# Optimization experiments

Measured on AMD Instinct MI355X. Metric: run time of the kernel, lower is better.

The kernel has to match this reference:

```python
import jax, jax.numpy as jnp
import numpy as np

B, N, H, FE = 1024, 128, 128, 8  # jets batch, particles per jet, hidden, features+1


def setup_inputs() -> dict:
    key = jax.random.key(0)
    ks = jax.random.split(key, 6)
    s = 0.05  # small init scale to keep gates in a sane range
    return {
        "h": jax.random.normal(ks[0], (B, N, H), dtype=jnp.float32),
        "jets": jax.random.normal(ks[1], (B, N, FE), dtype=jnp.float32),
        "mask": jnp.ones((B, N), dtype=bool),  # unused by MPIdentity.forward, kept for signature parity
        "Wm": jax.random.normal(ks[2], (H, H), dtype=jnp.float32) * s,
        "bm": jnp.zeros((H,), dtype=jnp.float32),
        "W_ih": jax.random.normal(ks[3], (3 * H, H + FE), dtype=jnp.float32) * s,
        "W_hh": jax.random.normal(ks[4], (3 * H, H), dtype=jnp.float32) * s,
        "b_ih": jnp.zeros((3 * H,), dtype=jnp.float32),
        "b_hh": jnp.zeros((3 * H,), dtype=jnp.float32),
    }


def reference(h, jets, mask, Wm, bm, W_ih, W_hh, b_ih, b_hh):
    # DTNNMessage: linear hidden->hidden (nn.Linear applies x @ W.T + b)
    msg = jnp.einsum("bnh,kh->bnk", h, Wm) + bm            # [B,N,H]
    # sum over particles, broadcast back (repeat), tanh activation
    dist = jnp.sum(msg, axis=1, keepdims=True)              # [B,1,H]
    message = jnp.tanh(jnp.broadcast_to(dist, h.shape))     # [B,N,H]
    # GRUUpdate: GRUCell on concat([message, jets]) with state h
    x = jnp.concatenate([message, jets], axis=-1)           # [B,N,H+FE]
    gi = jnp.einsum("bnf,gf->bng", x, W_ih) + b_ih          # [B,N,3H]
    gh = jnp.einsum("bnh,gh->bng", h, W_hh) + b_hh          # [B,N,3H]
    i_r, i_z, i_n = jnp.split(gi, 3, axis=-1)
    h_r, h_z, h_n = jnp.split(gh, 3, axis=-1)
    r = jax.nn.sigmoid(i_r + h_r)
    z = jax.nn.sigmoid(i_z + h_z)
    n = jnp.tanh(i_n + r * h_n)
    return (1.0 - z) * n + z * h                            # [B,N,H]
```

## Files before the change

### kernel.cpp

```cpp
#include <hip/hip_runtime.h>
#include <hip/hip_bf16.h>

#define B_   1024
#define N_   128
#define H_   128
#define FE_  8
#define G3_  384

typedef short s8v __attribute__((ext_vector_type(8)));
typedef float f4v __attribute__((ext_vector_type(4)));

__device__ __forceinline__ unsigned short f2bf(float x) {
    unsigned int u = __float_as_uint(x);
    u += 0x7fffu + ((u >> 16) & 1u);
    return (unsigned short)(u >> 16);
}
__device__ __forceinline__ float bf2f(unsigned short s) {
    return __uint_as_float(((unsigned int)s) << 16);
}

__global__ __launch_bounds__(256) void k1_prep(
    const float* __restrict__ h, const float* __restrict__ Wm,
    const float* __restrict__ bm, const float* __restrict__ W_ih,
    const float* __restrict__ W_hh, const float* __restrict__ b_ih,
    float* __restrict__ gi_base,
    unsigned short* __restrict__ Whi, unsigned short* __restrict__ Wlo,
    unsigned short* __restrict__ Wth, unsigned short* __restrict__ Wtl)
{
    const int b = blockIdx.x;
    const int t = threadIdx.x;

    if (t < 51) {
        const int i = b * 51 + t;
        if (i < 49152) {
            const float x = W_hh[i];
            const unsigned short hb = f2bf(x);
            Whi[i] = hb;
            Wlo[i] = f2bf(x - bf2f(hb));
        } else {
            const int j = i - 49152;
            const float x = W_ih[(j >> 3) * 136 + 128 + (j & 7)];
            const unsigned short hb = f2bf(x);
            Wth[j] = hb;
            Wtl[j] = f2bf(x - bf2f(hb));
        }
    }

    __shared__ __align__(16) float4 part[256];
    __shared__ __align__(16) float  hsum[H_];
    __shared__ __align__(16) float  msg[H_];

    const float4* h4 = reinterpret_cast<const float4*>(h + (size_t)b * (N_ * H_));
    const int kc = t & 31;
    const int ng = t >> 5;
    float4 s = make_float4(0.f, 0.f, 0.f, 0.f);
    #pragma unroll
    for (int i = 0; i < 16; ++i) {
        float4 v = h4[(ng * 16 + i) * 32 + kc];
        s.x += v.x; s.y += v.y; s.z += v.z; s.w += v.w;
    }
    part[t] = s;
    __syncthreads();
    if (t < 32) {
        float4 a = part[t];
        #pragma unroll
        for (int g = 1; g < 8; ++g) {
            float4 v = part[g * 32 + t];
            a.x += v.x; a.y += v.y; a.z += v.z; a.w += v.w;
        }
        reinterpret_cast<float4*>(hsum)[t] = a;
    }
    __syncthreads();

    if (t < H_) {
        const float4* wr  = reinterpret_cast<const float4*>(Wm + t * H_);
        const float4* hs4 = reinterpret_cast<const float4*>(hsum);
        float d = 0.f;
        #pragma unroll
        for (int j = 0; j < 32; ++j) {
            float4 w = wr[j]; float4 x = hs4[j];
            d += w.x * x.x + w.y * x.y + w.z * x.z + w.w * x.w;
        }
        d += (float)N_ * bm[t];
        msg[t] = tanhf(d);
    }
    __syncthreads();

    for (int g = t; g < G3_; g += 256) {
        const float4* wr = reinterpret_cast<const float4*>(W_ih + g * (H_ + FE_));
        const float4* m4 = reinterpret_cast<const float4*>(msg);
        float d = 0.f;
        #pragma unroll
        for (int j = 0; j < 32; ++j) {
            float4 w = wr[j]; float4 x = m4[j];
            d += w.x * x.x + w.y * x.y + w.z * x.z + w.w * x.w;
        }
        gi_base[b * G3_ + g] = d + b_ih[g];
    }
}

__global__ __launch_bounds__(512, 4) void k2_mfma(
    const float* __restrict__ h, const float* __restrict__ jets,
    const unsigned short* __restrict__ Whi, const unsigned short* __restrict__ Wlo,
    const unsigned short* __restrict__ Wth, const unsigned short* __restrict__ Wtl,
    const float* __restrict__ b_hh, const float* __restrict__ gi_base,
    float* __restrict__ out)
{
    __shared__ __align__(16) unsigned short Ah[64 * H_];
    __shared__ __align__(16) unsigned short Al[64 * H_];

    const int t    = threadIdx.x;
    const int row0 = blockIdx.x * 64;
    const int b    = row0 >> 7;
    const int wv   = t >> 6;
    const int l    = t & 63;
    const int lr   = l & 15;
    const int lq   = l >> 4;
    const int col  = wv * 16 + lr;

    {
        const int r  = t >> 3;
        const int kq = (t & 7) * 16;
        const float4* src = reinterpret_cast<const float4*>(
            h + (size_t)(row0 + r) * H_ + kq);
        float xs[16];
        #pragma unroll
        for (int i = 0; i < 4; ++i) {
            const float4 v = src[i];
            xs[i * 4 + 0] = v.x; xs[i * 4 + 1] = v.y;
            xs[i * 4 + 2] = v.z; xs[i * 4 + 3] = v.w;
        }
        #pragma unroll
        for (int c = 0; c < 2; ++c) {
            s8v hv8, lv8;
            #pragma unroll
            for (int e = 0; e < 8; ++e) {
                const float x = xs[c * 8 + e];
                const unsigned short hb = f2bf(x);
                hv8[e] = (short)hb;
                lv8[e] = (short)f2bf(x - bf2f(hb));
            }
            const int s = ((kq >> 3) + c) ^ (r & 7);
            *reinterpret_cast<s8v*>(&Ah[r * H_ + s * 8]) = hv8;
            *reinterpret_cast<s8v*>(&Al[r * H_ + s * 8]) = lv8;
        }
    }
    __syncthreads();

    float gb[3], bh3[3];
    #pragma unroll
    for (int g = 0; g < 3; ++g) {
        gb[g]  = gi_base[b * G3_ + (g << 7) + col];
        bh3[g] = b_hh[(g << 7) + col];
    }

    #pragma unroll
    for (int rp = 0; rp < 2; ++rp) {
        f4v acc[2][3];
        f4v accT[2];
        #pragma unroll
        for (int rt = 0; rt < 2; ++rt) {
            #pragma unroll
            for (int g = 0; g < 3; ++g)
                #pragma unroll
                for (int e = 0; e < 4; ++e) acc[rt][g][e] = 0.f;
            #pragma unroll
            for (int e = 0; e < 4; ++e) accT[rt][e] = 0.f;
        }

        #pragma unroll
        for (int ks = 0; ks < 4; ++ks) {
            s8v aH[2], aL[2];
            #pragma unroll
            for (int rt = 0; rt < 2; ++rt) {
                const int r   = rp * 32 + rt * 16 + lr;
                const int idx = r * H_ + ((((ks << 2) + lq) ^ (r & 7)) << 3);
                aH[rt] = *reinterpret_cast<const s8v*>(&Ah[idx]);
                aL[rt] = *reinterpret_cast<const s8v*>(&Al[idx]);
            }
            #pragma unroll
            for (int g = 0; g < 3; ++g) {
                const int off = ((g << 7) + col) * H_ + ks * 32 + lq * 8;
                const s8v bH = *reinterpret_cast<const s8v*>(Whi + off);
                const s8v bL = *reinterpret_cast<const s8v*>(Wlo + off);
                #pragma unroll
                for (int rt = 0; rt < 2; ++rt) {
                    acc[rt][g] = __builtin_amdgcn_mfma_f32_16x16x32_bf16(
                        aH[rt], bH, acc[rt][g], 0, 0, 0);
                    acc[rt][g] = __builtin_amdgcn_mfma_f32_16x16x32_bf16(
                        aH[rt], bL, acc[rt][g], 0, 0, 0);
                    acc[rt][g] = __builtin_amdgcn_mfma_f32_16x16x32_bf16(
                        aL[rt], bH, acc[rt][g], 0, 0, 0);
                }
            }
        }

        s8v aTh[2], aTl[2];
        #pragma unroll
        for (int rt = 0; rt < 2; ++rt) {
            const int row = row0 + rp * 32 + rt * 16 + lr;
            const float4 j0 = *reinterpret_cast<const float4*>(jets + (size_t)row * FE_);
            const float4 j1 = *reinterpret_cast<const float4*>(jets + (size_t)row * FE_ + 4);
            const float jx[8] = {j0.x, j0.y, j0.z, j0.w, j1.x, j1.y, j1.z, j1.w};
            #pragma unroll
            for (int e = 0; e < 8; ++e) {
                const float x = (lq == 0) ? jx[e] : 0.f;
                const unsigned short hb = f2bf(x);
                aTh[rt][e] = (short)hb;
                aTl[rt][e] = (short)f2bf(x - bf2f(hb));
            }
        }
        #pragma unroll
        for (int g = 0; g < 3; ++g) {
            const int gi = (g << 7) + col;
            const s8v bTh = *reinterpret_cast<const s8v*>(Wth + gi * 8);
            const s8v bTl = *reinterpret_cast<const s8v*>(Wtl + gi * 8);
            #pragma unroll
            for (int rt = 0; rt < 2; ++rt) {
                if (g < 2) {
                    acc[rt][g] = __builtin_amdgcn_mfma_f32_16x16x32_bf16(
                        aTh[rt], bTh, acc[rt][g], 0, 0, 0);
                    acc[rt][g] = __builtin_amdgcn_mfma_f32_16x16x32_bf16(
                        aTh[rt], bTl, acc[rt][g], 0, 0, 0);
                    acc[rt][g] = __builtin_amdgcn_mfma_f32_16x16x32_bf16(
                        aTl[rt], bTh, acc[rt][g], 0, 0, 0);
                } else {
                    accT[rt] = __builtin_amdgcn_mfma_f32_16x16x32_bf16(
                        aTh[rt], bTh, accT[rt], 0, 0, 0);
                    accT[rt] = __builtin_amdgcn_mfma_f32_16x16x32_bf16(
                        aTh[rt], bTl, accT[rt], 0, 0, 0);
                    accT[rt] = __builtin_amdgcn_mfma_f32_16x16x32_bf16(
                        aTl[rt], bTh, accT[rt], 0, 0, 0);
                }
            }
        }

        #pragma unroll
        for (int rt = 0; rt < 2; ++rt) {
            #pragma unroll
            for (int ridx = 0; ridx < 4; ++ridx) {
                const int rl  = rp * 32 + rt * 16 + lq * 4 + ridx;
                const size_t row = (size_t)(row0 + rl);
                const float rr = 1.f / (1.f + __expf(-(gb[0] + bh3[0] + acc[rt][0][ridx])));
                const float zz = 1.f / (1.f + __expf(-(gb[1] + bh3[1] + acc[rt][1][ridx])));
                const float i_n = gb[2] + accT[rt][ridx];
                const float h_n = acc[rt][2][ridx] + bh3[2];
                const float e2  = __expf(2.f * (i_n + rr * h_n));
                const float nn  = 1.f - 2.f / (e2 + 1.f);
                const float hv  = h[row * H_ + col];
                out[row * H_ + col] = (1.f - zz) * nn + zz * hv;
            }
        }
    }
}

extern "C" void kernel_launch(void* const* d_in, const int* in_sizes, int n_in,
                              void* d_out, int out_size, void* d_ws, size_t ws_size,
                              hipStream_t stream) {
    const float* h    = (const float*)d_in[0];
    const float* jets = (const float*)d_in[1];
    const float* Wm   = (const float*)d_in[3];
    const float* bm   = (const float*)d_in[4];
    const float* W_ih = (const float*)d_in[5];
    const float* W_hh = (const float*)d_in[6];
    const float* b_ih = (const float*)d_in[7];
    const float* b_hh = (const float*)d_in[8];
    float* out = (float*)d_out;

    float* gi_base      = (float*)d_ws;
    unsigned short* Whi = (unsigned short*)((char*)d_ws + 1572864);
    unsigned short* Wlo = (unsigned short*)((char*)d_ws + 1671168);
    unsigned short* Wth = (unsigned short*)((char*)d_ws + 1769472);
    unsigned short* Wtl = (unsigned short*)((char*)d_ws + 1775616);

    k1_prep<<<dim3(B_), dim3(256), 0, stream>>>(h, Wm, bm, W_ih, W_hh, b_ih,
                                                gi_base, Whi, Wlo, Wth, Wtl);
    k2_mfma<<<dim3(B_ * N_ / 64), dim3(512), 0, stream>>>(h, jets, Whi, Wlo,
                                                          Wth, Wtl, b_hh,
                                                          gi_base, out);
}
```

Baseline: 263.7 us.

## Fuse message reduction and gate precompute into per-jet MFMA GRU kernel

Merges the per-jet reduction, message matvec and input-gate precompute into the main MFMA kernel, with one 512-thread block per jet. The column sum of h and the z*h term are rebuilt from the bf16 hi/lo copies already staged in LDS, so h is read from global memory only once. The weight split moves into a small separate kernel, and the global gi_base round trip is dropped. In exchange, LDS per block doubles, which may limit occupancy. The small matvecs now use wave shuffle reductions, and rebuilding h from hi+lo bf16 costs slight precision.

```diff
diff --git a/kernel.cpp b/kernel.cpp
--- a/kernel.cpp
+++ b/kernel.cpp
@@ -10,108 +10,53 @@
 typedef short s8v __attribute__((ext_vector_type(8)));
 typedef float f4v __attribute__((ext_vector_type(4)));
 
-__device__ __forceinline__ unsigned short f2bf(float x) {
+static __device__ __forceinline__ unsigned short f2bf(float x) {
     unsigned int u = __float_as_uint(x);
     u += 0x7fffu + ((u >> 16) & 1u);
     return (unsigned short)(u >> 16);
 }
-__device__ __forceinline__ float bf2f(unsigned short s) {
+static __device__ __forceinline__ float bf2f(unsigned short s) {
     return __uint_as_float(((unsigned int)s) << 16);
 }
 
-__global__ __launch_bounds__(256) void k1_prep(
-    const float* __restrict__ h, const float* __restrict__ Wm,
-    const float* __restrict__ bm, const float* __restrict__ W_ih,
-    const float* __restrict__ W_hh, const float* __restrict__ b_ih,
-    float* __restrict__ gi_base,
+__global__ __launch_bounds__(256) void k0_split(
+    const float* __restrict__ W_hh, const float* __restrict__ W_ih,
     unsigned short* __restrict__ Whi, unsigned short* __restrict__ Wlo,
     unsigned short* __restrict__ Wth, unsigned short* __restrict__ Wtl)
 {
-    const int b = blockIdx.x;
-    const int t = threadIdx.x;
-
-    if (t < 51) {
-        const int i = b * 51 + t;
-        if (i < 49152) {
-            const float x = W_hh[i];
-            const unsigned short hb = f2bf(x);
-            Whi[i] = hb;
-            Wlo[i] = f2bf(x - bf2f(hb));
-        } else {
-            const int j = i - 49152;
-            const float x = W_ih[(j >> 3) * 136 + 128 + (j & 7)];
-            const unsigned short hb = f2bf(x);
-            Wth[j] = hb;
-            Wtl[j] = f2bf(x - bf2f(hb));
-        }
-    }
-
-    __shared__ __align__(16) float4 part[256];
-    __shared__ __align__(16) float  hsum[H_];
-    __shared__ __align__(16) float  msg[H_];
-
-    const float4* h4 = reinterpret_cast<const float4*>(h + (size_t)b * (N_ * H_));
-    const int kc = t & 31;
-    const int ng = t >> 5;
-    float4 s = make_float4(0.f, 0.f, 0.f, 0.f);
-    #pragma unroll
-    for (int i = 0; i < 16; ++i) {
-        float4 v = h4[(ng * 16 + i) * 32 + kc];
-        s.x += v.x; s.y += v.y; s.z += v.z; s.w += v.w;
-    }
-    part[t] = s;
-    __syncthreads();
-    if (t < 32) {
-        float4 a = part[t];
-        #pragma unroll
-        for (int g = 1; g < 8; ++g) {
-            float4 v = part[g * 32 + t];
-            a.x += v.x; a.y += v.y; a.z += v.z; a.w += v.w;
-        }
-        reinterpret_cast<float4*>(hsum)[t] = a;
-    }
-    __syncthreads();
-
-    if (t < H_) {
-        const float4* wr  = reinterpret_cast<const float4*>(Wm + t * H_);
-        const float4* hs4 = reinterpret_cast<const float4*>(hsum);
-        float d = 0.f;
-        #pragma unroll
-        for (int j = 0; j < 32; ++j) {
-            float4 w = wr[j]; float4 x = hs4[j];
-            d += w.x * x.x + w.y * x.y + w.z * x.z + w.w * x.w;
-        }
-        d += (float)N_ * bm[t];
-        msg[t] = tanhf(d);
-    }
-    __syncthreads();
-
-    for (int g = t; g < G3_; g += 256) {
-        const float4* wr = reinterpret_cast<const float4*>(W_ih + g * (H_ + FE_));
-        const float4* m4 = reinterpret_cast<const float4*>(msg);
-        float d = 0.f;
-        #pragma unroll
-        for (int j = 0; j < 32; ++j) {
-            float4 w = wr[j]; float4 x = m4[j];
-            d += w.x * x.x + w.y * x.y + w.z * x.z + w.w * x.w;
-        }
-        gi_base[b * G3_ + g] = d + b_ih[g];
-    }
-}
-
-__global__ __launch_bounds__(512, 4) void k2_mfma(
+    const int i = blockIdx.x * 256 + threadIdx.x;
+    if (i < 49152) {
+        const float x = W_hh[i];
+        const unsigned short hb = f2bf(x);
+        Whi[i] = hb;
+        Wlo[i] = f2bf(x - bf2f(hb));
+    } else {
+        const int j = i - 49152;
+        const float x = W_ih[(j >> 3) * 136 + 128 + (j & 7)];
+        const unsigned short hb = f2bf(x);
+        Wth[j] = hb;
+        Wtl[j] = f2bf(x - bf2f(hb));
+    }
+}
+
+__global__ __launch_bounds__(512, 4) void k_fused(
     const float* __restrict__ h, const float* __restrict__ jets,
+    const float* __restrict__ Wm, const float* __restrict__ bm,
+    const float* __restrict__ W_ih, const float* __restrict__ b_ih,
     const unsigned short* __restrict__ Whi, const unsigned short* __restrict__ Wlo,
     const unsigned short* __restrict__ Wth, const unsigned short* __restrict__ Wtl,
-    const float* __restrict__ b_hh, const float* __restrict__ gi_base,
-    float* __restrict__ out)
+    const float* __restrict__ b_hh, float* __restrict__ out)
 {
-    __shared__ __align__(16) unsigned short Ah[64 * H_];
-    __shared__ __align__(16) unsigned short Al[64 * H_];
+    __shared__ __align__(16) unsigned short Ah[N_ * H_];
+    __shared__ __align__(16) unsigned short Al[N_ * H_];
+    __shared__ __align__(16) float red[512];
+    __shared__ __align__(16) float hsum_s[H_];
+    __shared__ __align__(16) float msg_s[H_];
+    __shared__ __align__(16) float gi_s[G3_];
 
     const int t    = threadIdx.x;
-    const int row0 = blockIdx.x * 64;
-    const int b    = row0 >> 7;
+    const int b    = blockIdx.x;
+    const int row0 = b * N_;
     const int wv   = t >> 6;
     const int l    = t & 63;
     const int lr   = l & 15;
@@ -119,30 +64,76 @@
     const int col  = wv * 16 + lr;
 
     {
-        const int r  = t >> 3;
+        const int rb = t >> 3;
         const int kq = (t & 7) * 16;
-        const float4* src = reinterpret_cast<const float4*>(
-            h + (size_t)(row0 + r) * H_ + kq);
-        float xs[16];
-        #pragma unroll
-        for (int i = 0; i < 4; ++i) {
-            const float4 v = src[i];
-            xs[i * 4 + 0] = v.x; xs[i * 4 + 1] = v.y;
-            xs[i * 4 + 2] = v.z; xs[i * 4 + 3] = v.w;
-        }
-        #pragma unroll
-        for (int c = 0; c < 2; ++c) {
-            s8v hv8, lv8;
-            #pragma unroll
-            for (int e = 0; e < 8; ++e) {
-                const float x = xs[c * 8 + e];
-                const unsigned short hb = f2bf(x);
-                hv8[e] = (short)hb;
-                lv8[e] = (short)f2bf(x - bf2f(hb));
-            }
-            const int s = ((kq >> 3) + c) ^ (r & 7);
-            *reinterpret_cast<s8v*>(&Ah[r * H_ + s * 8]) = hv8;
-            *reinterpret_cast<s8v*>(&Al[r * H_ + s * 8]) = lv8;
+        #pragma unroll
+        for (int half = 0; half < 2; ++half) {
+            const int r = rb + half * 64;
+            const float4* src = reinterpret_cast<const float4*>(
+                h + (size_t)(row0 + r) * H_ + kq);
+            float xs[16];
+            #pragma unroll
+            for (int i = 0; i < 4; ++i) {
+                const float4 v = src[i];
+                xs[i*4+0] = v.x; xs[i*4+1] = v.y; xs[i*4+2] = v.z; xs[i*4+3] = v.w;
+            }
+            #pragma unroll
+            for (int c = 0; c < 2; ++c) {
+                s8v hv8, lv8;
+                #pragma unroll
+                for (int e = 0; e < 8; ++e) {
+                    const float x = xs[c * 8 + e];
+                    const unsigned short hb = f2bf(x);
+                    hv8[e] = (short)hb;
+                    lv8[e] = (short)f2bf(x - bf2f(hb));
+                }
+                const int s = ((kq >> 3) + c) ^ (r & 7);
+                *reinterpret_cast<s8v*>(&Ah[r * H_ + s * 8]) = hv8;
+                *reinterpret_cast<s8v*>(&Al[r * H_ + s * 8]) = lv8;
+            }
+        }
+    }
+    __syncthreads();
+
+    {
+        const int c = t & 127, q = t >> 7;
+        float a = 0.f;
+        #pragma unroll 8
+        for (int i = 0; i < 32; ++i) {
+            const int r   = q * 32 + i;
+            const int idx = r * H_ + ((((c >> 3) ^ (r & 7)) << 3) + (c & 7));
+            a += bf2f(Ah[idx]) + bf2f(Al[idx]);
+        }
+        red[q * 128 + c] = a;
+    }
+    __syncthreads();
+    if (t < 128) hsum_s[t] = red[t] + red[128 + t] + red[256 + t] + red[384 + t];
+    __syncthreads();
+
+    {
+        const float2 hs2 = make_float2(hsum_s[2 * l], hsum_s[2 * l + 1]);
+        for (int i = 0; i < 16; ++i) {
+            const int g = wv * 16 + i;
+            const float2 w = *reinterpret_cast<const float2*>(Wm + g * H_ + 2 * l);
+            float d = hs2.x * w.x + hs2.y * w.y;
+            d += __shfl_xor(d, 1);  d += __shfl_xor(d, 2);
+            d += __shfl_xor(d, 4);  d += __shfl_xor(d, 8);
+            d += __shfl_xor(d, 16); d += __shfl_xor(d, 32);
+            if (l == 0) msg_s[g] = tanhf(d + (float)N_ * bm[g]);
+        }
+    }
+    __syncthreads();
+
+    {
+        const float2 ms2 = make_float2(msg_s[2 * l], msg_s[2 * l + 1]);
+        for (int i = 0; i < 48; ++i) {
+            const int g = wv * 48 + i;
+            const float2 w = *reinterpret_cast<const float2*>(W_ih + g * 136 + 2 * l);
+            float d = ms2.x * w.x + ms2.y * w.y;
+            d += __shfl_xor(d, 1);  d += __shfl_xor(d, 2);
+            d += __shfl_xor(d, 4);  d += __shfl_xor(d, 8);
+            d += __shfl_xor(d, 16); d += __shfl_xor(d, 32);
+            if (l == 0) gi_s[g] = d + b_ih[g];
         }
     }
     __syncthreads();
@@ -150,12 +141,12 @@
     float gb[3], bh3[3];
     #pragma unroll
     for (int g = 0; g < 3; ++g) {
-        gb[g]  = gi_base[b * G3_ + (g << 7) + col];
+        gb[g]  = gi_s[(g << 7) + col];
         bh3[g] = b_hh[(g << 7) + col];
     }
 
     #pragma unroll
-    for (int rp = 0; rp < 2; ++rp) {
+    for (int rp = 0; rp < 4; ++rp) {
         f4v acc[2][3];
         f4v accT[2];
         #pragma unroll
@@ -239,16 +230,16 @@
         for (int rt = 0; rt < 2; ++rt) {
             #pragma unroll
             for (int ridx = 0; ridx < 4; ++ridx) {
-                const int rl  = rp * 32 + rt * 16 + lq * 4 + ridx;
-                const size_t row = (size_t)(row0 + rl);
+                const int rl = rp * 32 + rt * 16 + lq * 4 + ridx;
                 const float rr = 1.f / (1.f + __expf(-(gb[0] + bh3[0] + acc[rt][0][ridx])));
                 const float zz = 1.f / (1.f + __expf(-(gb[1] + bh3[1] + acc[rt][1][ridx])));
                 const float i_n = gb[2] + accT[rt][ridx];
                 const float h_n = acc[rt][2][ridx] + bh3[2];
                 const float e2  = __expf(2.f * (i_n + rr * h_n));
                 const float nn  = 1.f - 2.f / (e2 + 1.f);
-                const float hv  = h[row * H_ + col];
-                out[row * H_ + col] = (1.f - zz) * nn + zz * hv;
+                const int hidx  = rl * H_ + ((((col >> 3) ^ (rl & 7)) << 3) + (col & 7));
+                const float hv  = bf2f(Ah[hidx]) + bf2f(Al[hidx]);
+                out[(size_t)(row0 + rl) * H_ + col] = (1.f - zz) * nn + zz * hv;
             }
         }
     }
@@ -267,15 +258,12 @@
     const float* b_hh = (const float*)d_in[8];
     float* out = (float*)d_out;
 
-    float* gi_base      = (float*)d_ws;
-    unsigned short* Whi = (unsigned short*)((char*)d_ws + 1572864);
-    unsigned short* Wlo = (unsigned short*)((char*)d_ws + 1671168);
-    unsigned short* Wth = (unsigned short*)((char*)d_ws + 1769472);
-    unsigned short* Wtl = (unsigned short*)((char*)d_ws + 1775616);
-
-    k1_prep<<<dim3(B_), dim3(256), 0, stream>>>(h, Wm, bm, W_ih, W_hh, b_ih,
-                                                gi_base, Whi, Wlo, Wth, Wtl);
-    k2_mfma<<<dim3(B_ * N_ / 64), dim3(512), 0, stream>>>(h, jets, Whi, Wlo,
-                                                          Wth, Wtl, b_hh,
-                                                          gi_base, out);
-}
+    unsigned short* Whi = (unsigned short*)d_ws;
+    unsigned short* Wlo = (unsigned short*)((char*)d_ws + 98304);
+    unsigned short* Wth = (unsigned short*)((char*)d_ws + 196608);
+    unsigned short* Wtl = (unsigned short*)((char*)d_ws + 202752);
+
+    k0_split<<<dim3(204), dim3(256), 0, stream>>>(W_hh, W_ih, Whi, Wlo, Wth, Wtl);
+    k_fused<<<dim3(B_), dim3(512), 0, stream>>>(h, jets, Wm, bm, W_ih, b_ih,
+                                                Whi, Wlo, Wth, Wtl, b_hh, out);
+}
```

New measurement: 295.8 us. 1.12x slower.
